# Performance work log

Measured on AMD Instinct MI355X. Metric: run time of the kernel, lower is better.

The kernel has to match this reference:

```python
import jax, jax.numpy as jnp
import numpy as np

NORM_CLAMP = 1e-4  # matches torch .clamp(min=0.0001) on the pairwise norm


def _kernel_rbf(x, y, w):
    # x: [B, N, D], y: [B, M, D], w: [B, 1, 1]
    x2 = jnp.sum(x * x, axis=-1)                      # [B, N]
    y2 = jnp.sum(y * y, axis=-1)                      # [B, M]
    xy = jnp.einsum('bnd,bmd->bnm', x, y)             # [B, N, M]
    sq = x2[:, :, None] + y2[:, None, :] - 2.0 * xy
    norm = jnp.sqrt(jnp.maximum(sq, 0.0))
    norm = jnp.maximum(norm, NORM_CLAMP)              # [B, N, M]
    d = x.shape[-1]
    return jnp.exp(-w * norm / d)                     # w broadcasts [B,1,1]


def setup_inputs() -> dict:
    key = jax.random.key(0)
    k1, k2, k3 = jax.random.split(key, 3)
    B, N, D = 32, 256, 32
    x = jax.random.normal(k1, (B, N, D), dtype=jnp.float32)
    y = jax.random.normal(k2, (B, N, D), dtype=jnp.float32)
    w = jax.random.uniform(k3, (B, 1, 1), dtype=jnp.float32)  # per-batch RBF bandwidth (= 1/delta_st)
    return {"x": x, "y": y, "w": w}


def reference(x, y, w):
    # _loss_mmd: mean over batch of per-batch MMD^2 estimates
    k_xx = _kernel_rbf(x, x, w)
    k_yy = _kernel_rbf(y, y, w)
    k_xy = _kernel_rbf(x, y, w)
    per_batch = (k_xx.mean(axis=(1, 2)) + k_yy.mean(axis=(1, 2))
                 - 2.0 * k_xy.mean(axis=(1, 2)))
    return per_batch.mean()
```

## Files before the change

kernel.cpp:

```cpp
#include <hip/hip_runtime.h>
#include <math.h>

#define BB 32
#define NN 256
#define DD 32
#define TPB 256
#define BPB 36
#define NBLK (BB * BPB)
#define NPART NBLK

typedef short  bf16x8 __attribute__((ext_vector_type(8)));
typedef float  f32x4  __attribute__((ext_vector_type(4)));

__device__ __forceinline__ unsigned cvt_pk_bf16(float a, float b) {
    unsigned r;
    asm("v_cvt_pk_bf16_f32 %0, %1, %2" : "=v"(r) : "v"(a), "v"(b));
    return r;
}
__device__ __forceinline__ float fast_sqrt(float x) {
    float r;
    asm("v_sqrt_f32 %0, %1" : "=v"(r) : "v"(x));
    return r;
}
__device__ __forceinline__ float fast_exp2(float x) {
    float r;
    asm("v_exp_f32 %0, %1" : "=v"(r) : "v"(x));
    return r;
}

__global__ __launch_bounds__(TPB) void mmd_main(
    const float* __restrict__ x, const float* __restrict__ y,
    const float* __restrict__ w, float* __restrict__ partials) {
    const int blk = blockIdx.x;
    const int b   = blk / BPB;
    const int rem = blk - b * BPB;
    const int type = (rem >= 10) + (rem >= 20);
    int iq, jq;
    float weight;
    if (type == 2) {
        const int k = rem - 20;
        iq = k >> 2; jq = k & 3;
        weight = -2.0f;
    } else {
        const int k = rem - type * 10;
        iq = (k >= 4) + (k >= 7) + (k >= 9);
        jq = iq + k - ((9 * iq - iq * iq) >> 1);
        weight = (iq == jq) ? 1.0f : 2.0f;
    }
    const int tid  = threadIdx.x;
    const int wv   = tid >> 6;
    const int lane = tid & 63;

    const float* Abase = (type == 1) ? y : x;
    const float* Bbase = (type == 0) ? x : y;
    const float* Aq = Abase + ((size_t)b * NN + iq * 64) * DD;
    const float* Bq = Bbase + ((size_t)b * NN + jq * 64) * DD;

    __shared__ bf16x8 Ah[4 * 64], Al[4 * 64], Bh[4 * 64], Bl[4 * 64];
    __shared__ float a2s[64], b2s[64];

    #pragma unroll
    for (int u = 0; u < 2; ++u) {
        const int e   = tid + u * 256;
        const int row = e >> 3;
        const int kq  = e & 7;
        const int g   = kq >> 1;
        const int hw  = kq & 1;
        const int slot = (row >> 4) * 64 + g * 16 + (row & 15);
        {
            const float4 v = ((const float4*)Aq)[e];
            const unsigned h01 = cvt_pk_bf16(v.x, v.y);
            const unsigned h23 = cvt_pk_bf16(v.z, v.w);
            const float r0 = v.x - __uint_as_float(h01 << 16);
            const float r1 = v.y - __uint_as_float(h01 & 0xffff0000u);
            const float r2 = v.z - __uint_as_float(h23 << 16);
            const float r3 = v.w - __uint_as_float(h23 & 0xffff0000u);
            ((uint2*)&Ah[slot])[hw] = make_uint2(h01, h23);
            ((uint2*)&Al[slot])[hw] =
                make_uint2(cvt_pk_bf16(r0, r1), cvt_pk_bf16(r2, r3));
        }
        {
            const float4 v = ((const float4*)Bq)[e];
            const unsigned h01 = cvt_pk_bf16(v.x, v.y);
            const unsigned h23 = cvt_pk_bf16(v.z, v.w);
            const float r0 = v.x - __uint_as_float(h01 << 16);
            const float r1 = v.y - __uint_as_float(h01 & 0xffff0000u);
            const float r2 = v.z - __uint_as_float(h23 << 16);
            const float r3 = v.w - __uint_as_float(h23 & 0xffff0000u);
            ((uint2*)&Bh[slot])[hw] = make_uint2(h01, h23);
            ((uint2*)&Bl[slot])[hw] =
                make_uint2(cvt_pk_bf16(r0, r1), cvt_pk_bf16(r2, r3));
        }
    }
    if (tid < 128) {
        const int r = tid & 63;
        const float4* rp = (const float4*)((tid < 64 ? Aq : Bq) + (size_t)r * DD);
        float c0 = 0.f, c1 = 0.f, c2 = 0.f, c3 = 0.f;
        #pragma unroll
        for (int k = 0; k < DD / 4; ++k) {
            float4 v = rp[k];
            c0 = fmaf(v.x, v.x, c0);
            c1 = fmaf(v.y, v.y, c1);
            c2 = fmaf(v.z, v.z, c2);
            c3 = fmaf(v.w, v.w, c3);
        }
        (tid < 64 ? a2s : b2s)[r] = (c0 + c1) + (c2 + c3);
    }
    __syncthreads();

    const bf16x8 bh = Bh[wv * 64 + lane];
    const bf16x8 bl = Bl[wv * 64 + lane];
    const float  b2 = b2s[wv * 16 + (lane & 15)];
    const float  negw2 = -w[b] * (1.0f / (float)DD) * 1.44269504088896f;
    const bool   sym = (type < 2) && (iq == jq);
    const int    rowbase = (lane >> 4) * 4;
    const int    colr = lane & 15;

    float acc = 0.f;
    #pragma unroll
    for (int it = 0; it < 4; ++it) {
        const bf16x8 ah = Ah[it * 64 + lane];
        const bf16x8 al = Al[it * 64 + lane];
        f32x4 c = {0.f, 0.f, 0.f, 0.f};
        c = __builtin_amdgcn_mfma_f32_16x16x32_bf16(al, bh, c, 0, 0, 0);
        c = __builtin_amdgcn_mfma_f32_16x16x32_bf16(ah, bl, c, 0, 0, 0);
        c = __builtin_amdgcn_mfma_f32_16x16x32_bf16(ah, bh, c, 0, 0, 0);
        const f32x4 a2q = *(const f32x4*)&a2s[it * 16 + rowbase];
        const bool diagt = sym && (it == wv);
        #pragma unroll
        for (int r = 0; r < 4; ++r) {
            float sq = fmaf(-2.0f, c[r], a2q[r] + b2);
            if (diagt && (rowbase + r == colr)) sq = 0.f;
            sq = fmaxf(sq, 1e-8f);
            acc += fast_exp2(negw2 * fast_sqrt(sq));
        }
    }

    #pragma unroll
    for (int off = 32; off > 0; off >>= 1) acc += __shfl_down(acc, off, 64);
    __shared__ float red[4];
    if (lane == 0) red[wv] = acc;
    __syncthreads();
    if (tid == 0) {
        const float bsum = (red[0] + red[1]) + (red[2] + red[3]);
        const float scale = weight / ((float)NN * (float)NN * (float)BB);
        partials[blk] = bsum * scale;
    }
}

__global__ __launch_bounds__(256) void mmd_reduce(
    const float* __restrict__ partials, float* __restrict__ out) {
    double acc = 0.0;
    #pragma unroll
    for (int t = 0; t < 5; ++t) {
        const int idx = threadIdx.x + t * 256;
        if (idx < NPART) acc += (double)partials[idx];
    }
    #pragma unroll
    for (int off = 32; off > 0; off >>= 1) acc += __shfl_down(acc, off, 64);
    __shared__ double red[4];
    if ((threadIdx.x & 63) == 0) red[threadIdx.x >> 6] = acc;
    __syncthreads();
    if (threadIdx.x == 0)
        out[0] = (float)((red[0] + red[1]) + (red[2] + red[3]));
}

extern "C" void kernel_launch(void* const* d_in, const int* in_sizes, int n_in,
                              void* d_out, int out_size, void* d_ws, size_t ws_size,
                              hipStream_t stream) {
    const float* x = (const float*)d_in[0];
    const float* y = (const float*)d_in[1];
    const float* w = (const float*)d_in[2];
    float* out = (float*)d_out;
    float* partials = (float*)d_ws;

    mmd_main<<<NBLK, TPB, 0, stream>>>(x, y, w, partials);
    mmd_reduce<<<1, 256, 0, stream>>>(partials, out);
}
```

Measured before the change: 12.46 us.

## Fuse final reduction into main kernel via last-block atomic counters

Drops the separate reduce kernel. Each block publishes its partial sum and bumps a hierarchical atomic counter (per group of 64 blocks, then a global counter), and the last block to finish sums all partials and writes the output. This removes one kernel launch and its dependency gap, but adds a memset launch to clear the counters each call, plus atomics and fences.

```diff
diff --git a/kernel.cpp b/kernel.cpp
--- a/kernel.cpp
+++ b/kernel.cpp
@@ -7,7 +7,8 @@
 #define TPB 256
 #define BPB 36
 #define NBLK (BB * BPB)
-#define NPART NBLK
+#define NGRP 18
+#define CNT_OFF 2048
 
 typedef short  bf16x8 __attribute__((ext_vector_type(8)));
 typedef float  f32x4  __attribute__((ext_vector_type(4)));
@@ -30,7 +31,11 @@
 
 __global__ __launch_bounds__(TPB) void mmd_main(
     const float* __restrict__ x, const float* __restrict__ y,
-    const float* __restrict__ w, float* __restrict__ partials) {
+    const float* __restrict__ w, float* __restrict__ ws,
+    float* __restrict__ out) {
+    float* partials = ws;
+    unsigned* cnt = (unsigned*)(ws + CNT_OFF);
+
     const int blk = blockIdx.x;
     const int b   = blk / BPB;
     const int rem = blk - b * BPB;
@@ -141,28 +146,40 @@
     __shared__ float red[4];
     if (lane == 0) red[wv] = acc;
     __syncthreads();
+
+    unsigned flag_local = 0;
     if (tid == 0) {
         const float bsum = (red[0] + red[1]) + (red[2] + red[3]);
         const float scale = weight / ((float)NN * (float)NN * (float)BB);
         partials[blk] = bsum * scale;
+        __threadfence();
+        const unsigned og = __hip_atomic_fetch_add(
+            &cnt[blk >> 6], 1u, __ATOMIC_RELAXED, __HIP_MEMORY_SCOPE_AGENT);
+        if (og == 63u) {
+            const unsigned om = __hip_atomic_fetch_add(
+                &cnt[NGRP], 1u, __ATOMIC_RELAXED, __HIP_MEMORY_SCOPE_AGENT);
+            flag_local = (om == NGRP - 1) ? 1u : 0u;
+        }
     }
-}
-
-__global__ __launch_bounds__(256) void mmd_reduce(
-    const float* __restrict__ partials, float* __restrict__ out) {
-    double acc = 0.0;
-    #pragma unroll
-    for (int t = 0; t < 5; ++t) {
-        const int idx = threadIdx.x + t * 256;
-        if (idx < NPART) acc += (double)partials[idx];
+    if (tid < 64) {
+        const unsigned f =
+            (unsigned)__builtin_amdgcn_readfirstlane((int)flag_local);
+        if (f) {
+            __threadfence();
+            double s = 0.0;
+            #pragma unroll
+            for (int t = 0; t < NBLK / 64; ++t) {
+                const float p = __hip_atomic_load(
+                    &partials[lane + t * 64],
+                    __ATOMIC_RELAXED, __HIP_MEMORY_SCOPE_AGENT);
+                s += (double)p;
+            }
+            #pragma unroll
+            for (int off = 32; off > 0; off >>= 1)
+                s += __shfl_down(s, off, 64);
+            if (lane == 0) out[0] = (float)s;
+        }
     }
-    #pragma unroll
-    for (int off = 32; off > 0; off >>= 1) acc += __shfl_down(acc, off, 64);
-    __shared__ double red[4];
-    if ((threadIdx.x & 63) == 0) red[threadIdx.x >> 6] = acc;
-    __syncthreads();
-    if (threadIdx.x == 0)
-        out[0] = (float)((red[0] + red[1]) + (red[2] + red[3]));
 }
 
 extern "C" void kernel_launch(void* const* d_in, const int* in_sizes, int n_in,
@@ -172,8 +189,8 @@
     const float* y = (const float*)d_in[1];
     const float* w = (const float*)d_in[2];
     float* out = (float*)d_out;
-    float* partials = (float*)d_ws;
+    float* ws  = (float*)d_ws;
 
-    mmd_main<<<NBLK, TPB, 0, stream>>>(x, y, w, partials);
-    mmd_reduce<<<1, 256, 0, stream>>>(partials, out);
+    (void)hipMemsetAsync((char*)d_ws + CNT_OFF * sizeof(float), 0, 128, stream);
+    mmd_main<<<NBLK, TPB, 0, stream>>>(x, y, w, ws, out);
 }
```

New measurement: 33.12 us. +165.9%, slower.
